# Kernel tuning notes

Measured on AMD Instinct MI355X. Metric: run time of the kernel, lower is better.

The kernel has to match this reference:

```python
import jax, jax.numpy as jnp
import numpy as np
from jax import lax

B, M, T = 64, 90, 187
NNLS_ITERS = 500   # fixed-iteration FISTA projected-gradient NNLS (replaces scipy.optimize.nnls loop)
POWER_ITERS = 50
NEG = 0.33         # leaky_relu negative_slope in BrainNetCNN


def leaky(x):
    return jnp.where(x >= 0, x, NEG * x)


def setup_inputs() -> dict:
    key = jax.random.key(0)
    ks = jax.random.split(key, 18)
    f32 = jnp.float32
    def g(k, shape, scale=0.05):
        return jax.random.normal(k, shape, dtype=f32) * scale
    return {
        "x0_raw": jax.random.normal(ks[0], (B, M, T), dtype=f32),   # trunk output res0+res2
        "raw_x": jax.random.normal(ks[1], (B, M, T), dtype=f32),    # mel[:, 0]
        # BrainNetCNN(1, 90, 2) parameters (full-extent conv kernels stored without singleton dims)
        "cnn1_w": g(ks[2], (8, M)),   "cnn1_b": jnp.zeros((8,), f32),    # Conv2d(1,8,(1,90))
        "cnn2_w": g(ks[3], (8, M)),   "cnn2_b": jnp.zeros((8,), f32),    # Conv2d(1,8,(90,1))
        "cnn3_w": g(ks[4], (16, 8, M)), "cnn3_b": jnp.zeros((16,), f32), # Conv2d(8,16,(1,90))
        "cnn4_w": g(ks[5], (16, 8, M)), "cnn4_b": jnp.zeros((16,), f32), # Conv2d(8,16,(90,1))
        "e2n_w": g(ks[6], (16, M)),  "e2n_b": jnp.zeros((1,), f32),      # Conv2d(16,1,(1,90))
        "n2g_w": g(ks[7], (64, M)),  "n2g_b": jnp.zeros((64,), f32),     # Conv2d(1,64,(90,1))
        "d1_w": g(ks[8], (128, 64)), "d1_b": jnp.zeros((128,), f32),
        "d2_w": g(ks[9], (10, 128)), "d2_b": jnp.zeros((10,), f32),
        "d3_w": g(ks[10], (2, 10)),  "d3_b": jnp.zeros((2,), f32),
    }


def nnls_columns(x0_pred, raw_x):
    """Batched NNLS: for each (b, j) solve min_{w>=0} ||X[:, !=j] w - raw_x[b, j]||^2.
    X = x0_pred^T [B,T,M]. Column j is excluded via a mask (its coefficient is pinned to 0),
    which is equivalent to deleting the column. Returns A[b, j, m] with zero diagonal
    (matching torch: A[i, indx, j] = nnls(...); A = A.transpose(1,2))."""
    X = jnp.swapaxes(x0_pred, 1, 2)                    # [B,T,M]
    G = jnp.einsum('btm,btn->bmn', X, X)               # [B,M,M] Gram, shared over all j-problems
    C = jnp.einsum('btm,bjt->bjm', X, raw_x)           # [B,M(j),M] X^T b_j
    mask = 1.0 - jnp.eye(M, dtype=X.dtype)             # mask[j,m]: exclude column j
    # Lipschitz constant: top eigenvalue of G via power iteration (valid bound for masked subproblems)
    v = jnp.ones((G.shape[0], M), G.dtype)
    def pit(v, _):
        v = jnp.einsum('bmn,bn->bm', G, v)
        v = v / (jnp.linalg.norm(v, axis=1, keepdims=True) + 1e-12)
        return v, None
    v, _ = lax.scan(pit, v, None, length=POWER_ITERS)
    L = jnp.einsum('bm,bmn,bn->b', v, G, v) * 1.01 + 1e-8
    step = (1.0 / L)[:, None, None]
    w0 = jnp.zeros_like(C)
    def fista(carry, _):
        w, y, t = carry
        grad = (jnp.einsum('bmn,bjn->bjm', G, y) - C) * mask
        w1 = jnp.maximum(y - step * grad, 0.0)
        t1 = 0.5 * (1.0 + jnp.sqrt(1.0 + 4.0 * t * t))
        y1 = w1 + ((t - 1.0) / t1) * (w1 - w)
        return (w1, y1, t1), None
    (w, _, _), _ = lax.scan(fista, (w0, w0, jnp.float32(1.0)), None, length=NNLS_ITERS)
    return w  # [B, j, m], diag == 0


def brainnet_cnn(A, cnn1_w, cnn1_b, cnn2_w, cnn2_b, cnn3_w, cnn3_b, cnn4_w, cnn4_b,
                 e2n_w, e2n_b, n2g_w, n2g_b, d1_w, d1_b, d2_w, d2_b, d3_w, d3_b):
    # E2E layer 1: row conv broadcast over width + col conv broadcast over height
    a = jnp.einsum('bhw,ow->boh', A, cnn1_w) + cnn1_b[None, :, None]   # [B,8,90]
    b = jnp.einsum('bhw,oh->bow', A, cnn2_w) + cnn2_b[None, :, None]   # [B,8,90]
    o1 = leaky(a[:, :, :, None] + b[:, :, None, :])                    # [B,8,90,90]
    a2 = jnp.einsum('bchw,ocw->boh', o1, cnn3_w) + cnn3_b[None, :, None]
    b2 = jnp.einsum('bchw,och->bow', o1, cnn4_w) + cnn4_b[None, :, None]
    o2 = leaky(a2[:, :, :, None] + b2[:, :, None, :])                  # [B,16,90,90]
    e2n = leaky(jnp.einsum('bchw,cw->bh', o2, e2n_w) + e2n_b)          # [B,90]
    n2g = leaky(jnp.einsum('bh,oh->bo', e2n, n2g_w) + n2g_b)           # [B,64]
    h = leaky(n2g @ d1_w.T + d1_b)
    h = leaky(h @ d2_w.T + d2_b)
    return leaky(h @ d3_w.T + d3_b)                                    # [B,2]


def reference(x0_raw, raw_x, cnn1_w, cnn1_b, cnn2_w, cnn2_b, cnn3_w, cnn3_b, cnn4_w, cnn4_b,
              e2n_w, e2n_b, n2g_w, n2g_b, d1_w, d1_b, d2_w, d2_b, d3_w, d3_b):
    mean_v = jnp.mean(x0_raw, axis=(1, 2), keepdims=True)
    max_v = jnp.max(jnp.abs(x0_raw), axis=(1, 2), keepdims=True)
    x0_pred = (x0_raw - mean_v) / max_v
    # torch detaches NNLS inputs (.detach().numpy()); mirror with stop_gradient
    A = nnls_columns(lax.stop_gradient(x0_pred), lax.stop_gradient(raw_x))
    cls_pred = brainnet_cnn(A, cnn1_w, cnn1_b, cnn2_w, cnn2_b, cnn3_w, cnn3_b, cnn4_w, cnn4_b,
                            e2n_w, e2n_b, n2g_w, n2g_b, d1_w, d1_b, d2_w, d2_b, d3_w, d3_b)
    return (x0_pred[:, None, :, :], A, cls_pred)
```

## Files before the change

kernel.cpp:

```cpp
#include <hip/hip_runtime.h>
#include <math.h>


#define B_ 64
#define M_ 90
#define T_ 187
#define MP 96
#define NNLS_ITERS 500
#define POWER_ITERS 50
#define NEG_SLOPE 0.33f

#define MT_ (M_ * T_)
#define X0_OFF 0
#define A_OFF (B_ * MT_)
#define CLS_OFF (A_OFF + B_ * M_ * M_)

#define WS_G 0
#define WS_C (B_ * MP * MP)
#define WS_STEP (2 * B_ * MP * MP)
#define WS_W3R (WS_STEP + B_)
#define WS_W4R (WS_W3R + 16 * 8 * M_)

typedef float f32x4 __attribute__((ext_vector_type(4)));
typedef short s16x8 __attribute__((ext_vector_type(8)));

__device__ __forceinline__ float leaky(float x) {
    return x >= 0.f ? x : NEG_SLOPE * x;
}

#define TSTR 193
__global__ __launch_bounds__(256) void k_gc(const float* __restrict__ x0,
                                            const float* __restrict__ rawx,
                                            float* __restrict__ ws,
                                            float* __restrict__ out) {
    int b = blockIdx.x, nh = blockIdx.y, tid = threadIdx.x;
    __shared__ float Ps[MP * TSTR];
    __shared__ float Rs[48 * TSTR];
    __shared__ float rs[256], rm[256];

    const float* x = x0 + b * MT_;
    {
        float s = 0.f, mx = 0.f;
        for (int i = tid; i < MT_; i += 256) {
            float v = x[i];
            s += v;
            mx = fmaxf(mx, fabsf(v));
        }
        rs[tid] = s; rm[tid] = mx;
    }
    __syncthreads();
    for (int st = 128; st > 0; st >>= 1) {
        if (tid < st) {
            rs[tid] += rs[tid + st];
            rm[tid] = fmaxf(rm[tid], rm[tid + st]);
        }
        __syncthreads();
    }
    float mean = rs[0] / (float)MT_;
    float mv = rm[0];

    for (int i = tid; i < MP * TSTR; i += 256) Ps[i] = 0.f;
    for (int i = tid; i < 48 * TSTR; i += 256) Rs[i] = 0.f;
    __syncthreads();

    const float* R = rawx + b * MT_;
    float* o = out + X0_OFF + b * MT_;
    for (int i = tid; i < MT_; i += 256) {
        int m = i / T_, t = i - m * T_;
        float pv = (x[i] - mean) / mv;
        Ps[m * TSTR + t] = pv;
        if (nh == 0) o[i] = pv;
    }
    for (int i = tid; i < 48 * T_; i += 256) {
        int k = i / T_, t = i - k * T_;
        int r = nh * 48 + k;
        if (r < M_) Rs[k * TSTR + t] = R[r * T_ + t];
    }
    __syncthreads();

    int tn = tid & 15;
    int tm = tid >> 4;
    const float* pmp = &Ps[(tm * 6) * TSTR];
    const float* pnp = &Ps[(nh * 48 + tn * 3) * TSTR];
    const float* rnp = &Rs[(tn * 3) * TSTR];

    float accG[6][3], accC[6][3];
#pragma unroll
    for (int i = 0; i < 6; ++i)
#pragma unroll
        for (int k = 0; k < 3; ++k) { accG[i][k] = 0.f; accC[i][k] = 0.f; }

#pragma unroll 2
    for (int t = 0; t < T_; ++t) {
        float pm[6], pn[3], rn[3];
#pragma unroll
        for (int i = 0; i < 6; ++i) pm[i] = pmp[i * TSTR + t];
#pragma unroll
        for (int k = 0; k < 3; ++k) { pn[k] = pnp[k * TSTR + t]; rn[k] = rnp[k * TSTR + t]; }
#pragma unroll
        for (int i = 0; i < 6; ++i)
#pragma unroll
            for (int k = 0; k < 3; ++k) {
                accG[i][k] = fmaf(pm[i], pn[k], accG[i][k]);
                accC[i][k] = fmaf(pm[i], rn[k], accC[i][k]);
            }
    }

    float* G = ws + WS_G + b * MP * MP;
    float* C = ws + WS_C + b * MP * MP;
#pragma unroll
    for (int i = 0; i < 6; ++i)
#pragma unroll
        for (int k = 0; k < 3; ++k) {
            int m = tm * 6 + i;
            int n = nh * 48 + tn * 3 + k;
            G[m * MP + n] = accG[i][k];
            C[n * MP + m] = accC[i][k];
        }
}

__global__ __launch_bounds__(256) void k_prepack(const float* __restrict__ w3,
                                                 const float* __restrict__ w4,
                                                 float* __restrict__ ws) {
    int tid = threadIdx.x + blockIdx.x * 256;
    for (int i = tid; i < 16 * 8 * M_; i += 512) {
        int o = i & 15;
        int cw = i >> 4;
        int c = cw / M_;
        int w = cw % M_;
        ws[WS_W3R + i] = w3[(o * 8 + c) * M_ + w];
        ws[WS_W4R + i] = w4[(o * 8 + c) * M_ + w];
    }
}

#define GSTR 100
__global__ __launch_bounds__(64) void k_power(float* __restrict__ ws) {
    int b = blockIdx.x, lane = threadIdx.x;
    const float* Gg = ws + WS_G + b * MP * MP;
    __shared__ float Gs[MP * GSTR];
    __shared__ float vs[MP];

    for (int i = lane; i < MP * MP; i += 64) {
        int m = i / MP, n = i - m * MP;
        Gs[m * GSTR + n] = Gg[i];
    }
    vs[lane] = (lane < M_) ? 1.f : 0.f;
    if (lane < 32) vs[64 + lane] = (64 + lane < M_) ? 1.f : 0.f;

    const float4* g0 = (const float4*)&Gs[lane * GSTR];
    const float4* g1 = (const float4*)&Gs[(64 + (lane & 31)) * GSTR];
    const float4* v4 = (const float4*)vs;

    float r0 = 0.f, r1 = 0.f;
    for (int it = 0; it <= POWER_ITERS; ++it) {
        r0 = 0.f; r1 = 0.f;
#pragma unroll 6
        for (int k = 0; k < MP / 4; ++k) {
            float4 gv = g0[k];
            float4 vv = v4[k];
            r0 = fmaf(gv.x, vv.x, r0);
            r0 = fmaf(gv.y, vv.y, r0);
            r0 = fmaf(gv.z, vv.z, r0);
            r0 = fmaf(gv.w, vv.w, r0);
        }
        if (lane < 32) {
#pragma unroll 6
            for (int k = 0; k < MP / 4; ++k) {
                float4 gv = g1[k];
                float4 vv = v4[k];
                r1 = fmaf(gv.x, vv.x, r1);
                r1 = fmaf(gv.y, vv.y, r1);
                r1 = fmaf(gv.z, vv.z, r1);
                r1 = fmaf(gv.w, vv.w, r1);
            }
        }
        if (it == POWER_ITERS) break;
        float s = r0 * r0 + ((lane < 32) ? r1 * r1 : 0.f);
#pragma unroll
        for (int d = 1; d < 64; d <<= 1) s += __shfl_xor(s, d, 64);
        float inv = 1.f / (sqrtf(s) + 1e-12f);
        vs[lane] = r0 * inv;
        if (lane < 32) vs[64 + lane] = r1 * inv;
    }
    float s = vs[lane] * r0 + ((lane < 32) ? vs[64 + lane] * r1 : 0.f);
#pragma unroll
    for (int d = 1; d < 64; d <<= 1) s += __shfl_xor(s, d, 64);
    if (lane == 0) ws[WS_STEP + b] = 1.f / (s * 1.01f + 1e-8f);
}

#define YSTR 104

__global__ __launch_bounds__(384) void k_fista(const float* __restrict__ ws,
                                               float* __restrict__ out) {
    int b = blockIdx.y;
    int j0 = blockIdx.x * 16;
    int tid = threadIdx.x;
    int wid = tid >> 6;
    int lane = tid & 63;
    int jl = lane & 15;
    int g = lane >> 4;

    const float* Gg = ws + WS_G + b * MP * MP;
    const float* Cg = ws + WS_C + b * MP * MP;
    float step = ws[WS_STEP + b];

    __shared__ unsigned short Yt[2][2][16 * YSTR];

    for (int i = tid; i < 2 * 2 * 16 * YSTR / 2; i += 384)
        ((unsigned int*)Yt)[i] = 0u;

    s16x8 ghi[3], glo[3];
#pragma unroll
    for (int nc = 0; nc < 3; ++nc) {
        const float* src = Gg + (wid * 16 + jl) * MP + nc * 32 + g * 8;
        s16x8 h, l;
#pragma unroll
        for (int e = 0; e < 8; ++e) {
            float f = src[e];
            unsigned int hb = __float_as_uint(f) & 0xFFFF0000u;
            h[e] = (short)(hb >> 16);
            float lo = f - __uint_as_float(hb);
            l[e] = (short)(__float_as_uint(lo) >> 16);
        }
        ghi[nc] = h;
        glo[nc] = l;
    }

    float c[4], w[4], y[4];
    {
        const float* src = Cg + (j0 + jl) * MP + wid * 16 + g * 4;
#pragma unroll
        for (int r = 0; r < 4; ++r) {
            c[r] = src[r];
            w[r] = 0.f;
            y[r] = 0.f;
        }
    }

    const unsigned short* rb[2][2];
    unsigned short* wb[2][2];
#pragma unroll
    for (int bu = 0; bu < 2; ++bu)
#pragma unroll
        for (int hl = 0; hl < 2; ++hl) {
            rb[bu][hl] = &Yt[bu][hl][jl * YSTR + g * 8];
            wb[bu][hl] = &Yt[bu][hl][jl * YSTR + wid * 16 + g * 4];
        }

    float t = 1.f;
    __syncthreads();

#define FISTA_BODY(CUR, NXT)                                                   \
    {                                                                          \
        s16x8 yh[3], yl[3];                                                    \
        _Pragma("unroll")                                                      \
        for (int nc = 0; nc < 3; ++nc) {                                       \
            yh[nc] = *(const s16x8*)(rb[CUR][0] + nc * 32);                    \
            yl[nc] = *(const s16x8*)(rb[CUR][1] + nc * 32);                    \
        }                                                                      \
        float t1 = 0.5f * (1.f + sqrtf(1.f + 4.f * t * t));                    \
        float coef = (t - 1.f) / t1;                                           \
        t = t1;                                                                \
        f32x4 a1 = {0.f, 0.f, 0.f, 0.f};                                       \
        f32x4 a2 = {0.f, 0.f, 0.f, 0.f};                                       \
        f32x4 a3 = {0.f, 0.f, 0.f, 0.f};                                       \
        _Pragma("unroll")                                                      \
        for (int nc = 0; nc < 3; ++nc)                                         \
            a1 = __builtin_amdgcn_mfma_f32_16x16x32_bf16(ghi[nc], yh[nc], a1, 0, 0, 0); \
        _Pragma("unroll")                                                      \
        for (int nc = 0; nc < 3; ++nc)                                         \
            a2 = __builtin_amdgcn_mfma_f32_16x16x32_bf16(ghi[nc], yl[nc], a2, 0, 0, 0); \
        _Pragma("unroll")                                                      \
        for (int nc = 0; nc < 3; ++nc)                                         \
            a3 = __builtin_amdgcn_mfma_f32_16x16x32_bf16(glo[nc], yh[nc], a3, 0, 0, 0); \
        unsigned int hb[4], lb[4];                                             \
        _Pragma("unroll")                                                      \
        for (int r = 0; r < 4; ++r) {                                          \
            int mg = wid * 16 + g * 4 + r;                                     \
            float gr = (a1[r] + a2[r] + a3[r]) - c[r];                         \
            if (j0 + jl == mg) gr = 0.f;                                       \
            float w1v = fmaxf(fmaf(-step, gr, y[r]), 0.f);                     \
            float yn = fmaf(coef, w1v - w[r], w1v);                            \
            w[r] = w1v;                                                        \
            y[r] = yn;                                                         \
            hb[r] = __float_as_uint(yn) & 0xFFFF0000u;                         \
            float lo = yn - __uint_as_float(hb[r]);                            \
            lb[r] = __float_as_uint(lo);                                       \
        }                                                                      \
        unsigned int h0 = (hb[0] >> 16) | hb[1];                               \
        unsigned int h1 = (hb[2] >> 16) | hb[3];                               \
        unsigned int l0 = (lb[0] >> 16) | (lb[1] & 0xFFFF0000u);               \
        unsigned int l1 = (lb[2] >> 16) | (lb[3] & 0xFFFF0000u);               \
        *(uint2*)(wb[NXT][0]) = make_uint2(h0, h1);                            \
        *(uint2*)(wb[NXT][1]) = make_uint2(l0, l1);                            \
        __syncthreads();                                                       \
    }

    for (int it = 0; it < NNLS_ITERS / 2; ++it) {
        FISTA_BODY(0, 1)
        FISTA_BODY(1, 0)
    }
#undef FISTA_BODY

    int jg = j0 + jl;
#pragma unroll
    for (int r = 0; r < 4; ++r) {
        int mg = wid * 16 + g * 4 + r;
        if (jg < M_ && mg < M_)
            out[A_OFF + b * M_ * M_ + jg * M_ + mg] = w[r];
    }
}

__global__ __launch_bounds__(256) void k_cnn(
    const float* __restrict__ out_in, const float* __restrict__ ws,
    const float* __restrict__ c1w, const float* __restrict__ c1b,
    const float* __restrict__ c2w, const float* __restrict__ c2b,
    const float* __restrict__ c3b, const float* __restrict__ c4b,
    const float* __restrict__ e2nw, const float* __restrict__ e2nb,
    const float* __restrict__ n2gw, const float* __restrict__ n2gb,
    const float* __restrict__ d1w, const float* __restrict__ d1b,
    const float* __restrict__ d2w, const float* __restrict__ d2b,
    const float* __restrict__ d3w, const float* __restrict__ d3b,
    float* __restrict__ out) {
    int b = blockIdx.x, tid = threadIdx.x;
    __shared__ float A[M_][92];
    __shared__ float a1[8][92], b1[8][92];
    __shared__ float a2s[16][92], b2s[16][92];
    __shared__ float part[16][92];
    __shared__ float e2n[92], n2g[64], h1[128], h2[12];

    const float* Ag = out_in + A_OFF + b * M_ * M_;
    for (int i = tid; i < M_ * M_; i += 256) A[i / M_][i % M_] = Ag[i];
    __syncthreads();

    for (int q = tid; q < 8 * M_; q += 256) {
        int o = q & 7, h = q >> 3;
        float s = c1b[o];
#pragma unroll 2
        for (int wI = 0; wI < M_; ++wI) s = fmaf(A[h][wI], c1w[o * M_ + wI], s);
        a1[o][h] = s;
    }
    for (int q = tid; q < 8 * M_; q += 256) {
        int o = q & 7, wI = q >> 3;
        float s = c2b[o];
#pragma unroll 2
        for (int h = 0; h < M_; ++h) s = fmaf(A[h][wI], c2w[o * M_ + h], s);
        b1[o][wI] = s;
    }
    __syncthreads();

    const float4* w3r4 = (const float4*)(ws + WS_W3R);
    const float4* w4r4 = (const float4*)(ws + WS_W4R);
    for (int q = tid; q < 720; q += 256) {
        if (q < 360) {
            int oq = q & 3, h = q >> 2;
            float4 acc = make_float4(c3b[4 * oq], c3b[4 * oq + 1],
                                     c3b[4 * oq + 2], c3b[4 * oq + 3]);
#pragma unroll
            for (int ci = 0; ci < 8; ++ci) {
                float av = a1[ci][h];
                for (int wI = 0; wI < M_; ++wI) {
                    float o1v = leaky(av + b1[ci][wI]);
                    float4 wv = w3r4[(ci * M_ + wI) * 4 + oq];
                    acc.x = fmaf(o1v, wv.x, acc.x);
                    acc.y = fmaf(o1v, wv.y, acc.y);
                    acc.z = fmaf(o1v, wv.z, acc.z);
                    acc.w = fmaf(o1v, wv.w, acc.w);
                }
            }
            a2s[4 * oq + 0][h] = acc.x;
            a2s[4 * oq + 1][h] = acc.y;
            a2s[4 * oq + 2][h] = acc.z;
            a2s[4 * oq + 3][h] = acc.w;
        } else {
            int q2 = q - 360;
            int oq = q2 & 3, wI = q2 >> 2;
            float4 acc = make_float4(c4b[4 * oq], c4b[4 * oq + 1],
                                     c4b[4 * oq + 2], c4b[4 * oq + 3]);
#pragma unroll
            for (int ci = 0; ci < 8; ++ci) {
                float bv = b1[ci][wI];
                for (int h = 0; h < M_; ++h) {
                    float o1v = leaky(a1[ci][h] + bv);
                    float4 wv = w4r4[(ci * M_ + h) * 4 + oq];
                    acc.x = fmaf(o1v, wv.x, acc.x);
                    acc.y = fmaf(o1v, wv.y, acc.y);
                    acc.z = fmaf(o1v, wv.z, acc.z);
                    acc.w = fmaf(o1v, wv.w, acc.w);
                }
            }
            b2s[4 * oq + 0][wI] = acc.x;
            b2s[4 * oq + 1][wI] = acc.y;
            b2s[4 * oq + 2][wI] = acc.z;
            b2s[4 * oq + 3][wI] = acc.w;
        }
    }
    __syncthreads();

    for (int q = tid; q < 16 * M_; q += 256) {
        int ci = q & 15, h = q >> 4;
        float av = a2s[ci][h];
        float s = 0.f;
        for (int wI = 0; wI < M_; ++wI)
            s = fmaf(leaky(av + b2s[ci][wI]), e2nw[ci * M_ + wI], s);
        part[ci][h] = s;
    }
    __syncthreads();
    if (tid < M_) {
        float s = e2nb[0];
#pragma unroll
        for (int ci = 0; ci < 16; ++ci) s += part[ci][tid];
        e2n[tid] = leaky(s);
    }
    __syncthreads();
    if (tid < 64) {
        float s = n2gb[tid];
        for (int h = 0; h < M_; ++h) s = fmaf(e2n[h], n2gw[tid * M_ + h], s);
        n2g[tid] = leaky(s);
    }
    __syncthreads();
    if (tid < 128) {
        float s = d1b[tid];
        for (int k = 0; k < 64; ++k) s = fmaf(n2g[k], d1w[tid * 64 + k], s);
        h1[tid] = leaky(s);
    }
    __syncthreads();
    if (tid < 10) {
        float s = d2b[tid];
        for (int k = 0; k < 128; ++k) s = fmaf(h1[k], d2w[tid * 128 + k], s);
        h2[tid] = leaky(s);
    }
    __syncthreads();
    if (tid < 2) {
        float s = d3b[tid];
        for (int k = 0; k < 10; ++k) s = fmaf(h2[k], d3w[tid * 10 + k], s);
        out[CLS_OFF + b * 2 + tid] = leaky(s);
    }
}

extern "C" void kernel_launch(void* const* d_in, const int* in_sizes, int n_in,
                              void* d_out, int out_size, void* d_ws, size_t ws_size,
                              hipStream_t stream) {
    const float* x0 = (const float*)d_in[0];
    const float* rawx = (const float*)d_in[1];
    const float* c1w = (const float*)d_in[2];
    const float* c1b = (const float*)d_in[3];
    const float* c2w = (const float*)d_in[4];
    const float* c2b = (const float*)d_in[5];
    const float* c3w = (const float*)d_in[6];
    const float* c3b = (const float*)d_in[7];
    const float* c4w = (const float*)d_in[8];
    const float* c4b = (const float*)d_in[9];
    const float* e2nw = (const float*)d_in[10];
    const float* e2nb = (const float*)d_in[11];
    const float* n2gw = (const float*)d_in[12];
    const float* n2gb = (const float*)d_in[13];
    const float* d1w = (const float*)d_in[14];
    const float* d1b = (const float*)d_in[15];
    const float* d2w = (const float*)d_in[16];
    const float* d2b = (const float*)d_in[17];
    const float* d3w = (const float*)d_in[18];
    const float* d3b = (const float*)d_in[19];

    float* out = (float*)d_out;
    float* ws = (float*)d_ws;

    hipLaunchKernelGGL(k_gc, dim3(B_, 2), dim3(256), 0, stream, x0, rawx, ws, out);
    hipLaunchKernelGGL(k_prepack, dim3(2), dim3(256), 0, stream, c3w, c4w, ws);
    hipLaunchKernelGGL(k_power, dim3(B_), dim3(64), 0, stream, ws);
    hipLaunchKernelGGL(k_fista, dim3(MP / 16, B_), dim3(384), 0, stream, ws, out);
    hipLaunchKernelGGL(k_cnn, dim3(B_), dim3(256), 0, stream, out, ws,
                       c1w, c1b, c2w, c2b, c3b, c4b, e2nw, e2nb,
                       n2gw, n2gb, d1w, d1b, d2w, d2b, d3w, d3b, out);
}
```

Measured before the change: 713.7 us.

## Run FISTA per block on a single wave covering all M tiles, dropping barriers

The NNLS FISTA kernel now uses one 64-lane wave per block instead of six. That wave holds all six 16-row Gram tiles in registers and computes the full gradient itself, so the per-iteration block barrier and the double-buffered shared-memory exchange go away. The subtraction of C is folded into the accumulator init, and the diagonal exclusion becomes a multiplicative mask. Rounding of the split high part changes from truncation to round-to-nearest. In exchange each wave issues six times more serial MFMA work per iteration, uses much more register space, and leaves fewer waves resident per CU. Separately, the CNN kernel stages e2n weights in shared memory and adds unroll pragmas.

```diff
diff --git a/kernel.cpp b/kernel.cpp
--- a/kernel.cpp
+++ b/kernel.cpp
@@ -1,4 +1,5 @@
 #include <hip/hip_runtime.h>
+#include <hip/hip_bf16.h>
 #include <math.h>
 
 
@@ -190,125 +191,125 @@
 
 #define YSTR 104
 
-__global__ __launch_bounds__(384) void k_fista(const float* __restrict__ ws,
-                                               float* __restrict__ out) {
+__global__ __launch_bounds__(64, 1) void k_fista(const float* __restrict__ ws,
+                                                 float* __restrict__ out) {
     int b = blockIdx.y;
     int j0 = blockIdx.x * 16;
-    int tid = threadIdx.x;
-    int wid = tid >> 6;
-    int lane = tid & 63;
+    int lane = threadIdx.x;
     int jl = lane & 15;
     int g = lane >> 4;
 
     const float* Gg = ws + WS_G + b * MP * MP;
     const float* Cg = ws + WS_C + b * MP * MP;
     float step = ws[WS_STEP + b];
-
-    __shared__ unsigned short Yt[2][2][16 * YSTR];
-
-    for (int i = tid; i < 2 * 2 * 16 * YSTR / 2; i += 384)
+    float nstep = -step;
+
+    __shared__ unsigned short Yt[2][16 * YSTR];
+
+    for (int i = lane; i < 2 * 16 * YSTR / 2; i += 64)
         ((unsigned int*)Yt)[i] = 0u;
 
-    s16x8 ghi[3], glo[3];
-#pragma unroll
-    for (int nc = 0; nc < 3; ++nc) {
-        const float* src = Gg + (wid * 16 + jl) * MP + nc * 32 + g * 8;
-        s16x8 h, l;
-#pragma unroll
-        for (int e = 0; e < 8; ++e) {
-            float f = src[e];
-            unsigned int hb = __float_as_uint(f) & 0xFFFF0000u;
-            h[e] = (short)(hb >> 16);
-            float lo = f - __uint_as_float(hb);
-            l[e] = (short)(__float_as_uint(lo) >> 16);
-        }
-        ghi[nc] = h;
-        glo[nc] = l;
-    }
-
-    float c[4], w[4], y[4];
-    {
-        const float* src = Cg + (j0 + jl) * MP + wid * 16 + g * 4;
+    s16x8 ghi[6][3], glo[6][3];
+#pragma unroll
+    for (int mt = 0; mt < 6; ++mt)
+#pragma unroll
+        for (int nc = 0; nc < 3; ++nc) {
+            const float* src = Gg + (mt * 16 + jl) * MP + nc * 32 + g * 8;
+            s16x8 h, l;
+#pragma unroll
+            for (int e = 0; e < 8; ++e) {
+                float f = src[e];
+                unsigned int hb = __float_as_uint(f) & 0xFFFF0000u;
+                h[e] = (short)(hb >> 16);
+                float lo = f - __uint_as_float(hb);
+                l[e] = (short)(__float_as_uint(lo) >> 16);
+            }
+            ghi[mt][nc] = h;
+            glo[mt][nc] = l;
+        }
+
+    f32x4 negc[6], dm[6], w4[6], y4[6];
+#pragma unroll
+    for (int mt = 0; mt < 6; ++mt) {
+        const float* src = Cg + (j0 + jl) * MP + mt * 16 + g * 4;
 #pragma unroll
         for (int r = 0; r < 4; ++r) {
-            c[r] = src[r];
-            w[r] = 0.f;
-            y[r] = 0.f;
-        }
-    }
-
-    const unsigned short* rb[2][2];
-    unsigned short* wb[2][2];
-#pragma unroll
-    for (int bu = 0; bu < 2; ++bu)
-#pragma unroll
-        for (int hl = 0; hl < 2; ++hl) {
-            rb[bu][hl] = &Yt[bu][hl][jl * YSTR + g * 8];
-            wb[bu][hl] = &Yt[bu][hl][jl * YSTR + wid * 16 + g * 4];
-        }
+            negc[mt][r] = -src[r];
+            dm[mt][r] = (j0 + jl == mt * 16 + g * 4 + r) ? 0.f : 1.f;
+            w4[mt][r] = 0.f;
+            y4[mt][r] = 0.f;
+        }
+    }
+
+    const unsigned short* rbh = &Yt[0][jl * YSTR + g * 8];
+    const unsigned short* rbl = &Yt[1][jl * YSTR + g * 8];
+    unsigned short* wbh = &Yt[0][jl * YSTR + g * 4];
+    unsigned short* wbl = &Yt[1][jl * YSTR + g * 4];
 
     float t = 1.f;
     __syncthreads();
 
-#define FISTA_BODY(CUR, NXT)                                                   \
-    {                                                                          \
-        s16x8 yh[3], yl[3];                                                    \
-        _Pragma("unroll")                                                      \
-        for (int nc = 0; nc < 3; ++nc) {                                       \
-            yh[nc] = *(const s16x8*)(rb[CUR][0] + nc * 32);                    \
-            yl[nc] = *(const s16x8*)(rb[CUR][1] + nc * 32);                    \
-        }                                                                      \
-        float t1 = 0.5f * (1.f + sqrtf(1.f + 4.f * t * t));                    \
-        float coef = (t - 1.f) / t1;                                           \
-        t = t1;                                                                \
-        f32x4 a1 = {0.f, 0.f, 0.f, 0.f};                                       \
-        f32x4 a2 = {0.f, 0.f, 0.f, 0.f};                                       \
-        f32x4 a3 = {0.f, 0.f, 0.f, 0.f};                                       \
-        _Pragma("unroll")                                                      \
-        for (int nc = 0; nc < 3; ++nc)                                         \
-            a1 = __builtin_amdgcn_mfma_f32_16x16x32_bf16(ghi[nc], yh[nc], a1, 0, 0, 0); \
-        _Pragma("unroll")                                                      \
-        for (int nc = 0; nc < 3; ++nc)                                         \
-            a2 = __builtin_amdgcn_mfma_f32_16x16x32_bf16(ghi[nc], yl[nc], a2, 0, 0, 0); \
-        _Pragma("unroll")                                                      \
-        for (int nc = 0; nc < 3; ++nc)                                         \
-            a3 = __builtin_amdgcn_mfma_f32_16x16x32_bf16(glo[nc], yh[nc], a3, 0, 0, 0); \
-        unsigned int hb[4], lb[4];                                             \
-        _Pragma("unroll")                                                      \
-        for (int r = 0; r < 4; ++r) {                                          \
-            int mg = wid * 16 + g * 4 + r;                                     \
-            float gr = (a1[r] + a2[r] + a3[r]) - c[r];                         \
-            if (j0 + jl == mg) gr = 0.f;                                       \
-            float w1v = fmaxf(fmaf(-step, gr, y[r]), 0.f);                     \
-            float yn = fmaf(coef, w1v - w[r], w1v);                            \
-            w[r] = w1v;                                                        \
-            y[r] = yn;                                                         \
-            hb[r] = __float_as_uint(yn) & 0xFFFF0000u;                         \
-            float lo = yn - __uint_as_float(hb[r]);                            \
-            lb[r] = __float_as_uint(lo);                                       \
-        }                                                                      \
-        unsigned int h0 = (hb[0] >> 16) | hb[1];                               \
-        unsigned int h1 = (hb[2] >> 16) | hb[3];                               \
-        unsigned int l0 = (lb[0] >> 16) | (lb[1] & 0xFFFF0000u);               \
-        unsigned int l1 = (lb[2] >> 16) | (lb[3] & 0xFFFF0000u);               \
-        *(uint2*)(wb[NXT][0]) = make_uint2(h0, h1);                            \
-        *(uint2*)(wb[NXT][1]) = make_uint2(l0, l1);                            \
-        __syncthreads();                                                       \
-    }
-
-    for (int it = 0; it < NNLS_ITERS / 2; ++it) {
-        FISTA_BODY(0, 1)
-        FISTA_BODY(1, 0)
-    }
-#undef FISTA_BODY
+    for (int it = 0; it < NNLS_ITERS; ++it) {
+        s16x8 yh[3], yl[3];
+#pragma unroll
+        for (int nc = 0; nc < 3; ++nc) {
+            yh[nc] = *(const s16x8*)(rbh + nc * 32);
+            yl[nc] = *(const s16x8*)(rbl + nc * 32);
+        }
+
+        float t1 = 0.5f * (1.f + sqrtf(1.f + 4.f * t * t));
+        float coef = (t - 1.f) / t1;
+        t = t1;
+
+#pragma unroll
+        for (int mt = 0; mt < 6; ++mt) {
+            f32x4 a1 = negc[mt];
+            f32x4 a2 = {0.f, 0.f, 0.f, 0.f};
+            f32x4 a3 = {0.f, 0.f, 0.f, 0.f};
+#pragma unroll
+            for (int nc = 0; nc < 3; ++nc)
+                a1 = __builtin_amdgcn_mfma_f32_16x16x32_bf16(ghi[mt][nc], yh[nc], a1, 0, 0, 0);
+#pragma unroll
+            for (int nc = 0; nc < 3; ++nc)
+                a2 = __builtin_amdgcn_mfma_f32_16x16x32_bf16(ghi[mt][nc], yl[nc], a2, 0, 0, 0);
+#pragma unroll
+            for (int nc = 0; nc < 3; ++nc)
+                a3 = __builtin_amdgcn_mfma_f32_16x16x32_bf16(glo[mt][nc], yh[nc], a3, 0, 0, 0);
+
+            f32x4 gr = (a1 + a2 + a3) * dm[mt];
+#pragma unroll
+            for (int r = 0; r < 4; ++r) {
+                float w1v = fmaxf(fmaf(nstep, gr[r], y4[mt][r]), 0.f);
+                float yn = fmaf(coef, w1v - w4[mt][r], w1v);
+                w4[mt][r] = w1v;
+                y4[mt][r] = yn;
+            }
+            __hip_bfloat162 hp0 = __float22bfloat162_rn(make_float2(y4[mt][0], y4[mt][1]));
+            __hip_bfloat162 hp1 = __float22bfloat162_rn(make_float2(y4[mt][2], y4[mt][3]));
+            unsigned int h0 = *reinterpret_cast<unsigned int*>(&hp0);
+            unsigned int h1 = *reinterpret_cast<unsigned int*>(&hp1);
+            float l0f = y4[mt][0] - __uint_as_float(h0 << 16);
+            float l1f = y4[mt][1] - __uint_as_float(h0 & 0xFFFF0000u);
+            float l2f = y4[mt][2] - __uint_as_float(h1 << 16);
+            float l3f = y4[mt][3] - __uint_as_float(h1 & 0xFFFF0000u);
+            __hip_bfloat162 lp0 = __float22bfloat162_rn(make_float2(l0f, l1f));
+            __hip_bfloat162 lp1 = __float22bfloat162_rn(make_float2(l2f, l3f));
+            *(uint2*)(wbh + mt * 16) = make_uint2(h0, h1);
+            *(uint2*)(wbl + mt * 16) =
+                make_uint2(*reinterpret_cast<unsigned int*>(&lp0),
+                           *reinterpret_cast<unsigned int*>(&lp1));
+        }
+    }
 
     int jg = j0 + jl;
 #pragma unroll
-    for (int r = 0; r < 4; ++r) {
-        int mg = wid * 16 + g * 4 + r;
-        if (jg < M_ && mg < M_)
-            out[A_OFF + b * M_ * M_ + jg * M_ + mg] = w[r];
-    }
+    for (int mt = 0; mt < 6; ++mt)
+#pragma unroll
+        for (int r = 0; r < 4; ++r) {
+            int mg = mt * 16 + g * 4 + r;
+            if (jg < M_ && mg < M_)
+                out[A_OFF + b * M_ * M_ + jg * M_ + mg] = w4[mt][r];
+        }
 }
 
 __global__ __launch_bounds__(256) void k_cnn(
@@ -327,23 +328,25 @@
     __shared__ float a1[8][92], b1[8][92];
     __shared__ float a2s[16][92], b2s[16][92];
     __shared__ float part[16][92];
+    __shared__ float sE2n[16][92];
     __shared__ float e2n[92], n2g[64], h1[128], h2[12];
 
     const float* Ag = out_in + A_OFF + b * M_ * M_;
     for (int i = tid; i < M_ * M_; i += 256) A[i / M_][i % M_] = Ag[i];
+    for (int i = tid; i < 16 * M_; i += 256) sE2n[i / M_][i % M_] = e2nw[i];
     __syncthreads();
 
     for (int q = tid; q < 8 * M_; q += 256) {
         int o = q & 7, h = q >> 3;
         float s = c1b[o];
-#pragma unroll 2
+#pragma unroll 3
         for (int wI = 0; wI < M_; ++wI) s = fmaf(A[h][wI], c1w[o * M_ + wI], s);
         a1[o][h] = s;
     }
     for (int q = tid; q < 8 * M_; q += 256) {
         int o = q & 7, wI = q >> 3;
         float s = c2b[o];
-#pragma unroll 2
+#pragma unroll 3
         for (int h = 0; h < M_; ++h) s = fmaf(A[h][wI], c2w[o * M_ + h], s);
         b1[o][wI] = s;
     }
@@ -359,6 +362,7 @@
 #pragma unroll
             for (int ci = 0; ci < 8; ++ci) {
                 float av = a1[ci][h];
+#pragma unroll 3
                 for (int wI = 0; wI < M_; ++wI) {
                     float o1v = leaky(av + b1[ci][wI]);
                     float4 wv = w3r4[(ci * M_ + wI) * 4 + oq];
@@ -380,6 +384,7 @@
 #pragma unroll
             for (int ci = 0; ci < 8; ++ci) {
                 float bv = b1[ci][wI];
+#pragma unroll 3
                 for (int h = 0; h < M_; ++h) {
                     float o1v = leaky(a1[ci][h] + bv);
                     float4 wv = w4r4[(ci * M_ + h) * 4 + oq];
@@ -401,8 +406,9 @@
         int ci = q & 15, h = q >> 4;
         float av = a2s[ci][h];
         float s = 0.f;
+#pragma unroll 3
         for (int wI = 0; wI < M_; ++wI)
-            s = fmaf(leaky(av + b2s[ci][wI]), e2nw[ci * M_ + wI], s);
+            s = fmaf(leaky(av + b2s[ci][wI]), sE2n[ci][wI], s);
         part[ci][h] = s;
     }
     __syncthreads();
@@ -415,24 +421,28 @@
     __syncthreads();
     if (tid < 64) {
         float s = n2gb[tid];
+#pragma unroll 3
         for (int h = 0; h < M_; ++h) s = fmaf(e2n[h], n2gw[tid * M_ + h], s);
         n2g[tid] = leaky(s);
     }
     __syncthreads();
     if (tid < 128) {
         float s = d1b[tid];
+#pragma unroll 4
         for (int k = 0; k < 64; ++k) s = fmaf(n2g[k], d1w[tid * 64 + k], s);
         h1[tid] = leaky(s);
     }
     __syncthreads();
     if (tid < 10) {
         float s = d2b[tid];
+#pragma unroll 4
         for (int k = 0; k < 128; ++k) s = fmaf(h1[k], d2w[tid * 128 + k], s);
         h2[tid] = leaky(s);
     }
     __syncthreads();
     if (tid < 2) {
         float s = d3b[tid];
+#pragma unroll
         for (int k = 0; k < 10; ++k) s = fmaf(h2[k], d3w[tid * 10 + k], s);
         out[CLS_OFF + b * 2 + tid] = leaky(s);
     }
@@ -468,7 +478,7 @@
     hipLaunchKernelGGL(k_gc, dim3(B_, 2), dim3(256), 0, stream, x0, rawx, ws, out);
     hipLaunchKernelGGL(k_prepack, dim3(2), dim3(256), 0, stream, c3w, c4w, ws);
     hipLaunchKernelGGL(k_power, dim3(B_), dim3(64), 0, stream, ws);
-    hipLaunchKernelGGL(k_fista, dim3(MP / 16, B_), dim3(384), 0, stream, ws, out);
+    hipLaunchKernelGGL(k_fista, dim3(MP / 16, B_), dim3(64), 0, stream, ws, out);
     hipLaunchKernelGGL(k_cnn, dim3(B_), dim3(256), 0, stream, out, ws,
                        c1w, c1b, c2w, c2b, c3b, c4b, e2nw, e2nb,
                        n2gw, n2gb, d1w, d1b, d2w, d2b, d3w, d3b, out);
```

Result: slower. 1.010 ms (+41.6%).
